# Kernel tuning notes

Measured on AMD Instinct MI355X. Metric: run time of the kernel, lower is better.

Reference implementation:

```python
import jax, jax.numpy as jnp
import numpy as np

E = 8        # n_experts
TOP_K = 2    # top_k_experts


def setup_inputs() -> dict:
    key = jax.random.key(0)
    ks = jax.random.split(key, 4)
    B, N, D, H = 4, 2048, 1024, 1024
    s_d = 1.0 / np.sqrt(D)
    s_h = 1.0 / np.sqrt(H)
    return {
        "x": jax.random.normal(ks[0], (B, N, D), dtype=jnp.float32),
        "router_w": jax.random.normal(ks[1], (E, D), dtype=jnp.float32) * s_d,
        "router_b": jnp.zeros((E,), dtype=jnp.float32),
        "W_up": jax.random.normal(ks[2], (E, D, H), dtype=jnp.float32) * s_d,
        "b_up": jnp.zeros((E, H), dtype=jnp.float32),
        "W_down": jax.random.normal(ks[3], (E, H, D), dtype=jnp.float32) * s_h,
        "b_down": jnp.zeros((E, D), dtype=jnp.float32),
    }


def reference(x, router_w, router_b, W_up, b_up, W_down, b_down):
    # Router logits: (B, N, E)
    logits = jnp.einsum("bnd,ed->bne", x, router_w) + router_b
    _, topk_idx = jax.lax.top_k(logits, TOP_K)          # (B, N, K)
    # Boolean mask of selected experts: (B, N, E)
    mask = jax.nn.one_hot(topk_idx, E, dtype=jnp.bool_).any(axis=-2)
    masked_logits = jnp.where(mask, logits, -jnp.inf)
    router_weights = jax.nn.softmax(masked_logits, axis=-1)  # zeros off top-k
    # Dense all-experts FFN: (B, N, E, H) intermediate
    h = jnp.einsum("bnd,edh->bneh", x, W_up) + b_up
    h = jax.nn.gelu(h, approximate=False)  # torch F.gelu default = exact erf
    h = jnp.einsum("bneh,ehd->bned", h, W_down) + b_down
    output = jnp.einsum("bne,bned->bnd", router_weights, h)
    # Switch load-balancing aux loss (dropout is identity in eval)
    f_i = mask.astype(x.dtype).mean(axis=(0, 1))
    P_i = router_weights.mean(axis=(0, 1))
    aux_loss = E * jnp.sum(f_i * P_i)
    return output, aux_loss
```

## Files before the change

kernel.cpp:

```cpp
#include <hip/hip_runtime.h>
#include <hip/hip_bf16.h>

typedef __attribute__((ext_vector_type(8))) short bf16x8_t;
typedef __attribute__((ext_vector_type(4))) float f32x4_t;

__device__ __forceinline__ void gld16(void* lds, const void* g) {
    __builtin_amdgcn_global_load_lds(
        (const __attribute__((address_space(1))) void*)g,
        (__attribute__((address_space(3))) void*)lds, 16, 0, 0);
}

__device__ inline unsigned short f2bf(float f) {
    __hip_bfloat16 h = __float2bfloat16(f);
    return *reinterpret_cast<unsigned short*>(&h);
}

__global__ __launch_bounds__(256) void transpose_kernel(
    const float* __restrict__ Wup, const float* __restrict__ Wdn,
    ushort* __restrict__ WtUp, ushort* __restrict__ WtDn)
{
    int z = blockIdx.z;
    const float* src = (z < 8) ? (Wup + ((size_t)z << 20)) : (Wdn + ((size_t)(z - 8) << 20));
    ushort* dst      = (z < 8) ? (WtUp + ((size_t)z << 20)) : (WtDn + ((size_t)(z - 8) << 20));
    __shared__ float tile[64][65];
    int x0 = blockIdx.x * 64, y0 = blockIdx.y * 64;
    int row = threadIdx.x >> 4, colq = threadIdx.x & 15;
#pragma unroll
    for (int it = 0; it < 4; it++) {
        int r = row + it * 16;
        float4 v = *(const float4*)(src + (size_t)(y0 + r) * 1024 + x0 + colq * 4);
        tile[r][colq * 4 + 0] = v.x; tile[r][colq * 4 + 1] = v.y;
        tile[r][colq * 4 + 2] = v.z; tile[r][colq * 4 + 3] = v.w;
    }
    __syncthreads();
#pragma unroll
    for (int it = 0; it < 4; it++) {
        int r = row + it * 16;
        ushort4 o;
        o.x = f2bf(tile[colq * 4 + 0][r]); o.y = f2bf(tile[colq * 4 + 1][r]);
        o.z = f2bf(tile[colq * 4 + 2][r]); o.w = f2bf(tile[colq * 4 + 3][r]);
        *(ushort4*)(dst + (size_t)(x0 + r) * 1024 + y0 + colq * 4) = o;
    }
}

__global__ __launch_bounds__(256) void router_kernel(
    const float* __restrict__ x, const float* __restrict__ rw,
    const float* __restrict__ rb, ushort* __restrict__ xb,
    int2* __restrict__ tok_e, float2* __restrict__ tok_w)
{
    int wave = threadIdx.x >> 6, lane = threadIdx.x & 63;
    int t = blockIdx.x * 4 + wave;
    float4 xv[4];
#pragma unroll
    for (int i = 0; i < 4; i++)
        xv[i] = *(const float4*)(x + (size_t)t * 1024 + i * 256 + lane * 4);
#pragma unroll
    for (int i = 0; i < 4; i++) {
        ushort4 o;
        o.x = f2bf(xv[i].x); o.y = f2bf(xv[i].y); o.z = f2bf(xv[i].z); o.w = f2bf(xv[i].w);
        *(ushort4*)(xb + (size_t)t * 1024 + i * 256 + lane * 4) = o;
    }
    float logit[8];
#pragma unroll
    for (int e = 0; e < 8; e++) {
        float s = 0.f;
#pragma unroll
        for (int i = 0; i < 4; i++) {
            float4 wv = *(const float4*)(rw + e * 1024 + i * 256 + lane * 4);
            s += xv[i].x * wv.x + xv[i].y * wv.y + xv[i].z * wv.z + xv[i].w * wv.w;
        }
#pragma unroll
        for (int m = 32; m >= 1; m >>= 1) s += __shfl_xor(s, m, 64);
        logit[e] = s + rb[e];
    }
    int i0 = 0;
#pragma unroll
    for (int e = 1; e < 8; e++) if (logit[e] > logit[i0]) i0 = e;
    int i1 = -1;
#pragma unroll
    for (int e = 0; e < 8; e++) if (e != i0 && (i1 < 0 || logit[e] > logit[i1])) i1 = e;
    float ev = expf(logit[i1] - logit[i0]);
    float s = 1.f + ev;
    if (lane == 0) {
        tok_e[t] = make_int2(i0, i1);
        tok_w[t] = make_float2(1.f / s, ev / s);
    }
}

__global__ __launch_bounds__(256) void count_kernel(
    const int2* __restrict__ tok_e, const float2* __restrict__ tok_w,
    int* __restrict__ blockCnt, float* __restrict__ blockSum)
{
    __shared__ int lcnt[8];
    __shared__ float lsum[8];
    int tid = threadIdx.x;
    if (tid < 8) { lcnt[tid] = 0; lsum[tid] = 0.f; }
    __syncthreads();
    int t = blockIdx.x * 256 + tid;
    int2 e = tok_e[t]; float2 w = tok_w[t];
    atomicAdd(&lcnt[e.x], 1); atomicAdd(&lsum[e.x], w.x);
    atomicAdd(&lcnt[e.y], 1); atomicAdd(&lsum[e.y], w.y);
    __syncthreads();
    if (tid < 8) {
        blockCnt[blockIdx.x * 8 + tid] = lcnt[tid];
        blockSum[blockIdx.x * 8 + tid] = lsum[tid];
    }
}

__global__ void scan_kernel(const int* __restrict__ blockCnt,
                            const float* __restrict__ blockSum,
                            int* __restrict__ cnt, int* __restrict__ off,
                            int* __restrict__ base, int* __restrict__ tileE,
                            int* __restrict__ tileRow, int* __restrict__ nTiles,
                            float* aux_out)
{
    if (threadIdx.x == 0) {
        int tot[8]; float sw[8];
        for (int e = 0; e < 8; e++) { tot[e] = 0; sw[e] = 0.f; }
        for (int b = 0; b < 32; b++)
            for (int e = 0; e < 8; e++) { tot[e] += blockCnt[b * 8 + e]; sw[e] += blockSum[b * 8 + e]; }
        int o = 0; float aux = 0.f; int nT = 0;
        for (int e = 0; e < 8; e++) {
            cnt[e] = tot[e]; off[e] = o;
            aux += (float)tot[e] * sw[e];
            int run = o;
            for (int b = 0; b < 32; b++) { base[b * 8 + e] = run; run += blockCnt[b * 8 + e]; }
            for (int tt = 0; tt * 128 < tot[e]; tt++) { tileE[nT] = e; tileRow[nT] = o + tt * 128; nT++; }
            o += tot[e];
        }
        *nTiles = nT;
        aux *= 8.0f / (8192.0f * 8192.0f);
        *aux_out = aux;
    }
}

__global__ __launch_bounds__(256) void assign_kernel(
    const int2* __restrict__ tok_e, const float2* __restrict__ tok_w,
    const int* __restrict__ base, int* __restrict__ pair_token,
    float* __restrict__ pair_w, int2* __restrict__ tokSlot)
{
    __shared__ int lcnt[8];
    int tid = threadIdx.x;
    if (tid < 8) lcnt[tid] = 0;
    __syncthreads();
    int t = blockIdx.x * 256 + tid;
    int2 e = tok_e[t]; float2 w = tok_w[t];
    int r0 = atomicAdd(&lcnt[e.x], 1);
    int r1 = atomicAdd(&lcnt[e.y], 1);
    int s0 = base[blockIdx.x * 8 + e.x] + r0;
    int s1 = base[blockIdx.x * 8 + e.y] + r1;
    pair_token[s0] = t; pair_w[s0] = w.x;
    pair_token[s1] = t; pair_w[s1] = w.y;
    tokSlot[t] = make_int2(s0, s1);
}

__global__ __launch_bounds__(512, 4) void up_gemm(
    const ushort* __restrict__ xb, const ushort* __restrict__ WtUp,
    const float* __restrict__ bup,
    const int* __restrict__ cnt, const int* __restrict__ off,
    const int* __restrict__ nTiles, const int* __restrict__ tileE,
    const int* __restrict__ tileRow,
    const int* __restrict__ pair_token, const float* __restrict__ pair_w,
    const ushort* __restrict__ zeroPage, ushort* __restrict__ Hbuf)
{
    if ((int)blockIdx.y >= *nTiles) return;
    int e = tileE[blockIdx.y];
    int rowBase = tileRow[blockIdx.y];
    int expertEnd = off[e] + cnt[e];
    int colBase = blockIdx.x * 128;
    const ushort* Bsrc = WtUp + ((size_t)e << 20);

    __shared__ ushort As[128 * 32];
    __shared__ ushort Bs[128 * 32];

    int tid = threadIdx.x, w = tid >> 6, lane = tid & 63;
    int q = lane >> 4, r = lane & 15;
    int wm = w & 3, wn = w >> 2;

    int sr = lane >> 2;
    int cOff = (lane & 3) * 8;
    int rA = w * 16 + sr;
    int gA = rowBase + rA;

    const ushort* aP = (gA < expertEnd) ? xb + (size_t)pair_token[gA] * 1024 + cOff : zeroPage + cOff;
    const ushort* bP = Bsrc + (size_t)(colBase + rA) * 1024 + cOff;

    ushort* lA = &As[(w * 16) * 32];
    ushort* lB = &Bs[(w * 16) * 32];

    f32x4_t acc[2][4];
#pragma unroll
    for (int i = 0; i < 2; i++)
#pragma unroll
        for (int j = 0; j < 4; j++) { acc[i][j][0] = 0.f; acc[i][j][1] = 0.f; acc[i][j][2] = 0.f; acc[i][j][3] = 0.f; }

    for (int kk = 0; kk < 1024; kk += 32) {
        gld16(lA, aP + kk);
        gld16(lB, bP + kk);
        __syncthreads();
        bf16x8_t a[2], b[4];
#pragma unroll
        for (int i = 0; i < 2; i++) a[i] = *(const bf16x8_t*)&As[(wm * 32 + i * 16 + r) * 32 + q * 8];
#pragma unroll
        for (int j = 0; j < 4; j++) b[j] = *(const bf16x8_t*)&Bs[(wn * 64 + j * 16 + r) * 32 + q * 8];
#pragma unroll
        for (int i = 0; i < 2; i++)
#pragma unroll
            for (int j = 0; j < 4; j++)
                acc[i][j] = __builtin_amdgcn_mfma_f32_16x16x32_bf16(a[i], b[j], acc[i][j], 0, 0, 0);
        __syncthreads();
    }

#pragma unroll
    for (int j = 0; j < 4; j++) {
        int col = colBase + wn * 64 + j * 16 + r;
        float bias = bup[e * 1024 + col];
#pragma unroll
        for (int i = 0; i < 2; i++) {
#pragma unroll
            for (int reg = 0; reg < 4; reg++) {
                int gRow = rowBase + wm * 32 + i * 16 + q * 4 + reg;
                if (gRow < expertEnd) {
                    float h = acc[i][j][reg] + bias;
                    float g = 0.5f * h * (1.0f + erff(h * 0.70710678118654752f));
                    Hbuf[(size_t)gRow * 1024 + col] = f2bf(g * pair_w[gRow]);
                }
            }
        }
    }
}

__global__ __launch_bounds__(512, 4) void down_gemm(
    const ushort* __restrict__ Hbuf, const ushort* __restrict__ WtDn,
    const int* __restrict__ cnt, const int* __restrict__ off,
    const int* __restrict__ nTiles, const int* __restrict__ tileE,
    const int* __restrict__ tileRow,
    const ushort* __restrict__ zeroPage, ushort* __restrict__ pairOut)
{
    if ((int)blockIdx.y >= *nTiles) return;
    int e = tileE[blockIdx.y];
    int rowBase = tileRow[blockIdx.y];
    int expertEnd = off[e] + cnt[e];
    int colBase = blockIdx.x * 128;
    const ushort* Bsrc = WtDn + ((size_t)e << 20);

    __shared__ ushort As[128 * 32];
    __shared__ ushort Bs[128 * 32];

    int tid = threadIdx.x, w = tid >> 6, lane = tid & 63;
    int q = lane >> 4, r = lane & 15;
    int wm = w & 3, wn = w >> 2;

    int sr = lane >> 2;
    int cOff = (lane & 3) * 8;
    int rA = w * 16 + sr;
    int gA = rowBase + rA;

    const ushort* aP = (gA < expertEnd) ? Hbuf + (size_t)gA * 1024 + cOff : zeroPage + cOff;
    const ushort* bP = Bsrc + (size_t)(colBase + rA) * 1024 + cOff;

    ushort* lA = &As[(w * 16) * 32];
    ushort* lB = &Bs[(w * 16) * 32];

    f32x4_t acc[2][4];
#pragma unroll
    for (int i = 0; i < 2; i++)
#pragma unroll
        for (int j = 0; j < 4; j++) { acc[i][j][0] = 0.f; acc[i][j][1] = 0.f; acc[i][j][2] = 0.f; acc[i][j][3] = 0.f; }

    for (int kk = 0; kk < 1024; kk += 32) {
        gld16(lA, aP + kk);
        gld16(lB, bP + kk);
        __syncthreads();
        bf16x8_t a[2], b[4];
#pragma unroll
        for (int i = 0; i < 2; i++) a[i] = *(const bf16x8_t*)&As[(wm * 32 + i * 16 + r) * 32 + q * 8];
#pragma unroll
        for (int j = 0; j < 4; j++) b[j] = *(const bf16x8_t*)&Bs[(wn * 64 + j * 16 + r) * 32 + q * 8];
#pragma unroll
        for (int i = 0; i < 2; i++)
#pragma unroll
            for (int j = 0; j < 4; j++)
                acc[i][j] = __builtin_amdgcn_mfma_f32_16x16x32_bf16(a[i], b[j], acc[i][j], 0, 0, 0);
        __syncthreads();
    }

#pragma unroll
    for (int j = 0; j < 4; j++) {
        int col = colBase + wn * 64 + j * 16 + r;
#pragma unroll
        for (int i = 0; i < 2; i++) {
#pragma unroll
            for (int reg = 0; reg < 4; reg++) {
                int gRow = rowBase + wm * 32 + i * 16 + q * 4 + reg;
                if (gRow < expertEnd)
                    pairOut[(size_t)gRow * 1024 + col] = f2bf(acc[i][j][reg]);
            }
        }
    }
}

__global__ __launch_bounds__(256) void finalize_kernel(
    const ushort* __restrict__ pairOut, const int2* __restrict__ tokSlot,
    const int2* __restrict__ tok_e, const float2* __restrict__ tok_w,
    const float* __restrict__ bdn, float* __restrict__ out)
{
    int t = blockIdx.x;
    int2 s = tokSlot[t]; int2 e = tok_e[t]; float2 w = tok_w[t];
    int c = threadIdx.x * 4;
    ushort4 p0 = *(const ushort4*)(pairOut + (size_t)s.x * 1024 + c);
    ushort4 p1 = *(const ushort4*)(pairOut + (size_t)s.y * 1024 + c);
    float4 b0 = *(const float4*)(bdn + (size_t)e.x * 1024 + c);
    float4 b1 = *(const float4*)(bdn + (size_t)e.y * 1024 + c);
    __hip_bfloat16* h0 = (__hip_bfloat16*)&p0;
    __hip_bfloat16* h1 = (__hip_bfloat16*)&p1;
    float4 o;
    o.x = __bfloat162float(h0[0]) + __bfloat162float(h1[0]) + w.x * b0.x + w.y * b1.x;
    o.y = __bfloat162float(h0[1]) + __bfloat162float(h1[1]) + w.x * b0.y + w.y * b1.y;
    o.z = __bfloat162float(h0[2]) + __bfloat162float(h1[2]) + w.x * b0.z + w.y * b1.z;
    o.w = __bfloat162float(h0[3]) + __bfloat162float(h1[3]) + w.x * b0.w + w.y * b1.w;
    *(float4*)(out + (size_t)t * 1024 + c) = o;
}

extern "C" void kernel_launch(void* const* d_in, const int* in_sizes, int n_in,
                              void* d_out, int out_size, void* d_ws, size_t ws_size,
                              hipStream_t stream) {
    const float* x   = (const float*)d_in[0];
    const float* rw  = (const float*)d_in[1];
    const float* rb  = (const float*)d_in[2];
    const float* Wup = (const float*)d_in[3];
    const float* bup = (const float*)d_in[4];
    const float* Wdn = (const float*)d_in[5];
    const float* bdn = (const float*)d_in[6];
    float* out = (float*)d_out;

    char* ws = (char*)d_ws;
    int*    cnt      = (int*)(ws + 0);
    int*    off      = (int*)(ws + 64);
    int*    nTiles   = (int*)(ws + 128);
    int*    blockCnt = (int*)(ws + 256);
    float*  blockSum = (float*)(ws + 1536);
    int*    base     = (int*)(ws + 2816);
    int*    tileE    = (int*)(ws + 4096);
    int*    tileRow  = (int*)(ws + 4736);
    ushort* zeroPage = (ushort*)(ws + 8192);
    int2*   tok_e    = (int2*)(ws + 12288);
    float2* tok_w    = (float2*)(ws + 77824);
    int2*   tokSlot  = (int2*)(ws + 143360);
    int*    pair_token = (int*)(ws + 208896);
    float*  pair_w     = (float*)(ws + 274432);
    char* big = ws + 1048576;
    ushort* Hbuf    = (ushort*)big;
    ushort* pairOut = (ushort*)(big + 33554432);
    ushort* WtUp    = (ushort*)(big + 67108864);
    ushort* WtDn    = (ushort*)(big + 83886080);
    ushort* xb      = (ushort*)(big + 100663296);

    hipMemsetAsync(zeroPage, 0, 4096, stream);

    transpose_kernel<<<dim3(16, 16, 16), 256, 0, stream>>>(Wup, Wdn, WtUp, WtDn);
    router_kernel<<<2048, 256, 0, stream>>>(x, rw, rb, xb, tok_e, tok_w);
    count_kernel<<<32, 256, 0, stream>>>(tok_e, tok_w, blockCnt, blockSum);
    scan_kernel<<<1, 64, 0, stream>>>(blockCnt, blockSum, cnt, off, base,
                                      tileE, tileRow, nTiles, out + 8388608);
    assign_kernel<<<32, 256, 0, stream>>>(tok_e, tok_w, base, pair_token, pair_w, tokSlot);
    up_gemm<<<dim3(8, 136), 512, 0, stream>>>(
        xb, WtUp, bup, cnt, off, nTiles, tileE, tileRow, pair_token, pair_w, zeroPage, Hbuf);
    down_gemm<<<dim3(8, 136), 512, 0, stream>>>(
        Hbuf, WtDn, cnt, off, nTiles, tileE, tileRow, zeroPage, pairOut);
    finalize_kernel<<<8192, 256, 0, stream>>>(pairOut, tokSlot, tok_e, tok_w, bdn, out);
}
```

Measured before the change: 344.4 us.

## Switch expert GEMMs to 32x32x16 MFMA with 4-wave blocks and K=64 tiles

Both grouped GEMMs now use 256-thread blocks of 4 waves, each computing a 64x64 sub-tile with 32x32x16 bf16 MFMA instead of 16x16x32. K steps double to 64 per LDS stage, which halves the barrier count, and the LDS layout is arranged in MFMA-fragment order so each lane reads its operand with one contiguous vector load. The aim is higher MFMA throughput per LDS read and less sync overhead. The costs are more accumulator registers per thread and fewer waves per block to hide latency. An empty unused template helper is also added.

```diff
diff --git a/kernel.cpp b/kernel.cpp
--- a/kernel.cpp
+++ b/kernel.cpp
@@ -2,7 +2,7 @@
 #include <hip/hip_bf16.h>
 
 typedef __attribute__((ext_vector_type(8))) short bf16x8_t;
-typedef __attribute__((ext_vector_type(4))) float f32x4_t;
+typedef __attribute__((ext_vector_type(16))) float f32x16_t;
 
 __device__ __forceinline__ void gld16(void* lds, const void* g) {
     __builtin_amdgcn_global_load_lds(
@@ -154,7 +154,13 @@
     tokSlot[t] = make_int2(s0, s1);
 }
 
-__global__ __launch_bounds__(512, 4) void up_gemm(
+
+template <bool UP>
+__device__ __forceinline__ void gemm128_body(
+    const ushort* __restrict__ Asrc_rows[],
+    int dummy) {}
+
+__global__ __launch_bounds__(256, 4) void up_gemm(
     const ushort* __restrict__ xb, const ushort* __restrict__ WtUp,
     const float* __restrict__ bup,
     const int* __restrict__ cnt, const int* __restrict__ off,
@@ -170,67 +176,74 @@
     int colBase = blockIdx.x * 128;
     const ushort* Bsrc = WtUp + ((size_t)e << 20);
 
-    __shared__ ushort As[128 * 32];
-    __shared__ ushort Bs[128 * 32];
+    __shared__ ushort As[128 * 64];
+    __shared__ ushort Bs[128 * 64];
 
     int tid = threadIdx.x, w = tid >> 6, lane = tid & 63;
-    int q = lane >> 4, r = lane & 15;
-    int wm = w & 3, wn = w >> 2;
-
-    int sr = lane >> 2;
-    int cOff = (lane & 3) * 8;
-    int rA = w * 16 + sr;
-    int gA = rowBase + rA;
-
-    const ushort* aP = (gA < expertEnd) ? xb + (size_t)pair_token[gA] * 1024 + cOff : zeroPage + cOff;
-    const ushort* bP = Bsrc + (size_t)(colBase + rA) * 1024 + cOff;
-
-    ushort* lA = &As[(w * 16) * 32];
-    ushort* lB = &Bs[(w * 16) * 32];
-
-    f32x4_t acc[2][4];
+    int half = lane >> 5, m = lane & 31;
+    int wm = w & 1, wn = w >> 1;
+
+    int gA = rowBase + w * 32 + m;
+    const ushort* aRow = (gA < expertEnd) ? xb + (size_t)pair_token[gA] * 1024 : zeroPage;
+    const ushort* aP = aRow + half * 8;
+    const ushort* bP = Bsrc + (size_t)(colBase + w * 32 + m) * 1024 + half * 8;
+    ushort* lA = &As[w * 2048];
+    ushort* lB = &Bs[w * 2048];
+
+    f32x16_t acc[2][2];
 #pragma unroll
     for (int i = 0; i < 2; i++)
 #pragma unroll
-        for (int j = 0; j < 4; j++) { acc[i][j][0] = 0.f; acc[i][j][1] = 0.f; acc[i][j][2] = 0.f; acc[i][j][3] = 0.f; }
-
-    for (int kk = 0; kk < 1024; kk += 32) {
-        gld16(lA, aP + kk);
-        gld16(lB, bP + kk);
+        for (int j = 0; j < 2; j++)
+#pragma unroll
+            for (int p = 0; p < 16; p++) acc[i][j][p] = 0.f;
+
+    for (int kk = 0; kk < 1024; kk += 64) {
+#pragma unroll
+        for (int j = 0; j < 4; j++) {
+            gld16(lA + j * 512, aP + kk + j * 16);
+            gld16(lB + j * 512, bP + kk + j * 16);
+        }
         __syncthreads();
-        bf16x8_t a[2], b[4];
-#pragma unroll
-        for (int i = 0; i < 2; i++) a[i] = *(const bf16x8_t*)&As[(wm * 32 + i * 16 + r) * 32 + q * 8];
-#pragma unroll
-        for (int j = 0; j < 4; j++) b[j] = *(const bf16x8_t*)&Bs[(wn * 64 + j * 16 + r) * 32 + q * 8];
-#pragma unroll
-        for (int i = 0; i < 2; i++)
-#pragma unroll
-            for (int j = 0; j < 4; j++)
-                acc[i][j] = __builtin_amdgcn_mfma_f32_16x16x32_bf16(a[i], b[j], acc[i][j], 0, 0, 0);
+#pragma unroll
+        for (int s = 0; s < 4; s++) {
+            bf16x8_t a[2], b[2];
+#pragma unroll
+            for (int i = 0; i < 2; i++)
+                a[i] = *(const bf16x8_t*)&As[(((wm * 2 + i) * 4 + s) * 64 + lane) * 8];
+#pragma unroll
+            for (int j = 0; j < 2; j++)
+                b[j] = *(const bf16x8_t*)&Bs[(((wn * 2 + j) * 4 + s) * 64 + lane) * 8];
+#pragma unroll
+            for (int i = 0; i < 2; i++)
+#pragma unroll
+                for (int j = 0; j < 2; j++)
+                    acc[i][j] = __builtin_amdgcn_mfma_f32_32x32x16_bf16(a[i], b[j], acc[i][j], 0, 0, 0);
+        }
         __syncthreads();
     }
 
 #pragma unroll
-    for (int j = 0; j < 4; j++) {
-        int col = colBase + wn * 64 + j * 16 + r;
-        float bias = bup[e * 1024 + col];
-#pragma unroll
-        for (int i = 0; i < 2; i++) {
-#pragma unroll
-            for (int reg = 0; reg < 4; reg++) {
-                int gRow = rowBase + wm * 32 + i * 16 + q * 4 + reg;
-                if (gRow < expertEnd) {
-                    float h = acc[i][j][reg] + bias;
+    for (int i = 0; i < 2; i++) {
+#pragma unroll
+        for (int p = 0; p < 16; p++) {
+            int rl = (p & 3) + 8 * (p >> 2) + 4 * half;
+            int gRow = rowBase + (wm * 2 + i) * 32 + rl;
+            if (gRow < expertEnd) {
+                float wgt = pair_w[gRow];
+#pragma unroll
+                for (int j = 0; j < 2; j++) {
+                    int col = colBase + (wn * 2 + j) * 32 + m;
+                    float h = acc[i][j][p] + bup[e * 1024 + col];
                     float g = 0.5f * h * (1.0f + erff(h * 0.70710678118654752f));
-                    Hbuf[(size_t)gRow * 1024 + col] = f2bf(g * pair_w[gRow]);
+                    Hbuf[(size_t)gRow * 1024 + col] = f2bf(g * wgt);
                 }
             }
         }
     }
 }
 
-__global__ __launch_bounds__(512, 4) void down_gemm(
+__global__ __launch_bounds__(256, 4) void down_gemm(
     const ushort* __restrict__ Hbuf, const ushort* __restrict__ WtDn,
     const int* __restrict__ cnt, const int* __restrict__ off,
     const int* __restrict__ nTiles, const int* __restrict__ tileE,
@@ -244,57 +257,65 @@
     int colBase = blockIdx.x * 128;
     const ushort* Bsrc = WtDn + ((size_t)e << 20);
 
-    __shared__ ushort As[128 * 32];
-    __shared__ ushort Bs[128 * 32];
+    __shared__ ushort As[128 * 64];
+    __shared__ ushort Bs[128 * 64];
 
     int tid = threadIdx.x, w = tid >> 6, lane = tid & 63;
-    int q = lane >> 4, r = lane & 15;
-    int wm = w & 3, wn = w >> 2;
-
-    int sr = lane >> 2;
-    int cOff = (lane & 3) * 8;
-    int rA = w * 16 + sr;
-    int gA = rowBase + rA;
-
-    const ushort* aP = (gA < expertEnd) ? Hbuf + (size_t)gA * 1024 + cOff : zeroPage + cOff;
-    const ushort* bP = Bsrc + (size_t)(colBase + rA) * 1024 + cOff;
-
-    ushort* lA = &As[(w * 16) * 32];
-    ushort* lB = &Bs[(w * 16) * 32];
-
-    f32x4_t acc[2][4];
+    int half = lane >> 5, m = lane & 31;
+    int wm = w & 1, wn = w >> 1;
+
+    int gA = rowBase + w * 32 + m;
+    const ushort* aRow = (gA < expertEnd) ? Hbuf + (size_t)gA * 1024 : zeroPage;
+    const ushort* aP = aRow + half * 8;
+    const ushort* bP = Bsrc + (size_t)(colBase + w * 32 + m) * 1024 + half * 8;
+    ushort* lA = &As[w * 2048];
+    ushort* lB = &Bs[w * 2048];
+
+    f32x16_t acc[2][2];
 #pragma unroll
     for (int i = 0; i < 2; i++)
 #pragma unroll
-        for (int j = 0; j < 4; j++) { acc[i][j][0] = 0.f; acc[i][j][1] = 0.f; acc[i][j][2] = 0.f; acc[i][j][3] = 0.f; }
-
-    for (int kk = 0; kk < 1024; kk += 32) {
-        gld16(lA, aP + kk);
-        gld16(lB, bP + kk);
+        for (int j = 0; j < 2; j++)
+#pragma unroll
+            for (int p = 0; p < 16; p++) acc[i][j][p] = 0.f;
+
+    for (int kk = 0; kk < 1024; kk += 64) {
+#pragma unroll
+        for (int j = 0; j < 4; j++) {
+            gld16(lA + j * 512, aP + kk + j * 16);
+            gld16(lB + j * 512, bP + kk + j * 16);
+        }
         __syncthreads();
-        bf16x8_t a[2], b[4];
-#pragma unroll
-        for (int i = 0; i < 2; i++) a[i] = *(const bf16x8_t*)&As[(wm * 32 + i * 16 + r) * 32 + q * 8];
-#pragma unroll
-        for (int j = 0; j < 4; j++) b[j] = *(const bf16x8_t*)&Bs[(wn * 64 + j * 16 + r) * 32 + q * 8];
-#pragma unroll
-        for (int i = 0; i < 2; i++)
-#pragma unroll
-            for (int j = 0; j < 4; j++)
-                acc[i][j] = __builtin_amdgcn_mfma_f32_16x16x32_bf16(a[i], b[j], acc[i][j], 0, 0, 0);
+#pragma unroll
+        for (int s = 0; s < 4; s++) {
+            bf16x8_t a[2], b[2];
+#pragma unroll
+            for (int i = 0; i < 2; i++)
+                a[i] = *(const bf16x8_t*)&As[(((wm * 2 + i) * 4 + s) * 64 + lane) * 8];
+#pragma unroll
+            for (int j = 0; j < 2; j++)
+                b[j] = *(const bf16x8_t*)&Bs[(((wn * 2 + j) * 4 + s) * 64 + lane) * 8];
+#pragma unroll
+            for (int i = 0; i < 2; i++)
+#pragma unroll
+                for (int j = 0; j < 2; j++)
+                    acc[i][j] = __builtin_amdgcn_mfma_f32_32x32x16_bf16(a[i], b[j], acc[i][j], 0, 0, 0);
+        }
         __syncthreads();
     }
 
 #pragma unroll
-    for (int j = 0; j < 4; j++) {
-        int col = colBase + wn * 64 + j * 16 + r;
-#pragma unroll
-        for (int i = 0; i < 2; i++) {
-#pragma unroll
-            for (int reg = 0; reg < 4; reg++) {
-                int gRow = rowBase + wm * 32 + i * 16 + q * 4 + reg;
-                if (gRow < expertEnd)
-                    pairOut[(size_t)gRow * 1024 + col] = f2bf(acc[i][j][reg]);
+    for (int i = 0; i < 2; i++) {
+#pragma unroll
+        for (int p = 0; p < 16; p++) {
+            int rl = (p & 3) + 8 * (p >> 2) + 4 * half;
+            int gRow = rowBase + (wm * 2 + i) * 32 + rl;
+            if (gRow < expertEnd) {
+#pragma unroll
+                for (int j = 0; j < 2; j++) {
+                    int col = colBase + (wn * 2 + j) * 32 + m;
+                    pairOut[(size_t)gRow * 1024 + col] = f2bf(acc[i][j][p]);
+                }
             }
         }
     }
@@ -364,9 +385,9 @@
     scan_kernel<<<1, 64, 0, stream>>>(blockCnt, blockSum, cnt, off, base,
                                       tileE, tileRow, nTiles, out + 8388608);
     assign_kernel<<<32, 256, 0, stream>>>(tok_e, tok_w, base, pair_token, pair_w, tokSlot);
-    up_gemm<<<dim3(8, 136), 512, 0, stream>>>(
+    up_gemm<<<dim3(8, 136), 256, 0, stream>>>(
         xb, WtUp, bup, cnt, off, nTiles, tileE, tileRow, pair_token, pair_w, zeroPage, Hbuf);
-    down_gemm<<<dim3(8, 136), 512, 0, stream>>>(
+    down_gemm<<<dim3(8, 136), 256, 0, stream>>>(
         Hbuf, WtDn, cnt, off, nTiles, tileE, tileRow, zeroPage, pairOut);
     finalize_kernel<<<8192, 256, 0, stream>>>(pairOut, tokSlot, tok_e, tok_w, bdn, out);
 }
```

Measured after the change: 399.0 us. 15.8% more time.

## Swizzle LDS tiles, use tanh GELU, fold down bias into GEMM epilogue

Applied to the files above, without the earlier changes.

XOR-swizzles the 16-byte chunks of each LDS row in both expert GEMMs so that MFMA operand reads hit different banks, aiming to reduce LDS bank conflicts. Replaces the erf-based GELU with a tanh/exp approximation to cut epilogue cost, at the price of small numerical deviation from the exact GELU. Moves the weighted down-projection bias add into the down_gemm epilogue so the finalize kernel reads less data.

```diff
diff --git a/kernel.cpp b/kernel.cpp
--- a/kernel.cpp
+++ b/kernel.cpp
@@ -13,6 +13,11 @@
 __device__ inline unsigned short f2bf(float f) {
     __hip_bfloat16 h = __float2bfloat16(f);
     return *reinterpret_cast<unsigned short*>(&h);
+}
+
+__device__ __forceinline__ float gelu_fast(float h) {
+    float u = 0.7978845608028654f * h * (1.0f + 0.044715f * h * h);
+    return h / (1.0f + __expf(-2.0f * u));
 }
 
 __global__ __launch_bounds__(256) void transpose_kernel(
@@ -154,6 +159,7 @@
     tokSlot[t] = make_int2(s0, s1);
 }
 
+
 __global__ __launch_bounds__(512, 4) void up_gemm(
     const ushort* __restrict__ xb, const ushort* __restrict__ WtUp,
     const float* __restrict__ bup,
@@ -178,15 +184,16 @@
     int wm = w & 3, wn = w >> 2;
 
     int sr = lane >> 2;
-    int cOff = (lane & 3) * 8;
-    int rA = w * 16 + sr;
-    int gA = rowBase + rA;
+    int rowL = w * 16 + sr;
+    int qg = (lane & 3) ^ (sr & 3);
+    int cOff = qg * 8;
+    int gA = rowBase + rowL;
 
     const ushort* aP = (gA < expertEnd) ? xb + (size_t)pair_token[gA] * 1024 + cOff : zeroPage + cOff;
-    const ushort* bP = Bsrc + (size_t)(colBase + rA) * 1024 + cOff;
-
-    ushort* lA = &As[(w * 16) * 32];
-    ushort* lB = &Bs[(w * 16) * 32];
+    const ushort* bP = Bsrc + (size_t)(colBase + rowL) * 1024 + cOff;
+
+    ushort* lA = &As[w * 512];
+    ushort* lB = &Bs[w * 512];
 
     f32x4_t acc[2][4];
 #pragma unroll
@@ -200,9 +207,15 @@
         __syncthreads();
         bf16x8_t a[2], b[4];
 #pragma unroll
-        for (int i = 0; i < 2; i++) a[i] = *(const bf16x8_t*)&As[(wm * 32 + i * 16 + r) * 32 + q * 8];
-#pragma unroll
-        for (int j = 0; j < 4; j++) b[j] = *(const bf16x8_t*)&Bs[(wn * 64 + j * 16 + r) * 32 + q * 8];
+        for (int i = 0; i < 2; i++) {
+            int ra = wm * 32 + i * 16 + r;
+            a[i] = *(const bf16x8_t*)&As[ra * 32 + ((q ^ (ra & 3)) * 8)];
+        }
+#pragma unroll
+        for (int j = 0; j < 4; j++) {
+            int rb2 = wn * 64 + j * 16 + r;
+            b[j] = *(const bf16x8_t*)&Bs[rb2 * 32 + ((q ^ (rb2 & 3)) * 8)];
+        }
 #pragma unroll
         for (int i = 0; i < 2; i++)
 #pragma unroll
@@ -222,8 +235,7 @@
                 int gRow = rowBase + wm * 32 + i * 16 + q * 4 + reg;
                 if (gRow < expertEnd) {
                     float h = acc[i][j][reg] + bias;
-                    float g = 0.5f * h * (1.0f + erff(h * 0.70710678118654752f));
-                    Hbuf[(size_t)gRow * 1024 + col] = f2bf(g * pair_w[gRow]);
+                    Hbuf[(size_t)gRow * 1024 + col] = f2bf(gelu_fast(h) * pair_w[gRow]);
                 }
             }
         }
@@ -232,9 +244,10 @@
 
 __global__ __launch_bounds__(512, 4) void down_gemm(
     const ushort* __restrict__ Hbuf, const ushort* __restrict__ WtDn,
+    const float* __restrict__ bdn,
     const int* __restrict__ cnt, const int* __restrict__ off,
     const int* __restrict__ nTiles, const int* __restrict__ tileE,
-    const int* __restrict__ tileRow,
+    const int* __restrict__ tileRow, const float* __restrict__ pair_w,
     const ushort* __restrict__ zeroPage, ushort* __restrict__ pairOut)
 {
     if ((int)blockIdx.y >= *nTiles) return;
@@ -252,15 +265,16 @@
     int wm = w & 3, wn = w >> 2;
 
     int sr = lane >> 2;
-    int cOff = (lane & 3) * 8;
-    int rA = w * 16 + sr;
-    int gA = rowBase + rA;
+    int rowL = w * 16 + sr;
+    int qg = (lane & 3) ^ (sr & 3);
+    int cOff = qg * 8;
+    int gA = rowBase + rowL;
 
     const ushort* aP = (gA < expertEnd) ? Hbuf + (size_t)gA * 1024 + cOff : zeroPage + cOff;
-    const ushort* bP = Bsrc + (size_t)(colBase + rA) * 1024 + cOff;
-
-    ushort* lA = &As[(w * 16) * 32];
-    ushort* lB = &Bs[(w * 16) * 32];
+    const ushort* bP = Bsrc + (size_t)(colBase + rowL) * 1024 + cOff;
+
+    ushort* lA = &As[w * 512];
+    ushort* lB = &Bs[w * 512];
 
     f32x4_t acc[2][4];
 #pragma unroll
@@ -274,9 +288,15 @@
         __syncthreads();
         bf16x8_t a[2], b[4];
 #pragma unroll
-        for (int i = 0; i < 2; i++) a[i] = *(const bf16x8_t*)&As[(wm * 32 + i * 16 + r) * 32 + q * 8];
-#pragma unroll
-        for (int j = 0; j < 4; j++) b[j] = *(const bf16x8_t*)&Bs[(wn * 64 + j * 16 + r) * 32 + q * 8];
+        for (int i = 0; i < 2; i++) {
+            int ra = wm * 32 + i * 16 + r;
+            a[i] = *(const bf16x8_t*)&As[ra * 32 + ((q ^ (ra & 3)) * 8)];
+        }
+#pragma unroll
+        for (int j = 0; j < 4; j++) {
+            int rb2 = wn * 64 + j * 16 + r;
+            b[j] = *(const bf16x8_t*)&Bs[rb2 * 32 + ((q ^ (rb2 & 3)) * 8)];
+        }
 #pragma unroll
         for (int i = 0; i < 2; i++)
 #pragma unroll
@@ -288,13 +308,14 @@
 #pragma unroll
     for (int j = 0; j < 4; j++) {
         int col = colBase + wn * 64 + j * 16 + r;
+        float bias = bdn[e * 1024 + col];
 #pragma unroll
         for (int i = 0; i < 2; i++) {
 #pragma unroll
             for (int reg = 0; reg < 4; reg++) {
                 int gRow = rowBase + wm * 32 + i * 16 + q * 4 + reg;
                 if (gRow < expertEnd)
-                    pairOut[(size_t)gRow * 1024 + col] = f2bf(acc[i][j][reg]);
+                    pairOut[(size_t)gRow * 1024 + col] = f2bf(acc[i][j][reg] + pair_w[gRow] * bias);
             }
         }
     }
@@ -302,23 +323,20 @@
 
 __global__ __launch_bounds__(256) void finalize_kernel(
     const ushort* __restrict__ pairOut, const int2* __restrict__ tokSlot,
-    const int2* __restrict__ tok_e, const float2* __restrict__ tok_w,
-    const float* __restrict__ bdn, float* __restrict__ out)
+    float* __restrict__ out)
 {
     int t = blockIdx.x;
-    int2 s = tokSlot[t]; int2 e = tok_e[t]; float2 w = tok_w[t];
+    int2 s = tokSlot[t];
     int c = threadIdx.x * 4;
     ushort4 p0 = *(const ushort4*)(pairOut + (size_t)s.x * 1024 + c);
     ushort4 p1 = *(const ushort4*)(pairOut + (size_t)s.y * 1024 + c);
-    float4 b0 = *(const float4*)(bdn + (size_t)e.x * 1024 + c);
-    float4 b1 = *(const float4*)(bdn + (size_t)e.y * 1024 + c);
     __hip_bfloat16* h0 = (__hip_bfloat16*)&p0;
     __hip_bfloat16* h1 = (__hip_bfloat16*)&p1;
     float4 o;
-    o.x = __bfloat162float(h0[0]) + __bfloat162float(h1[0]) + w.x * b0.x + w.y * b1.x;
-    o.y = __bfloat162float(h0[1]) + __bfloat162float(h1[1]) + w.x * b0.y + w.y * b1.y;
-    o.z = __bfloat162float(h0[2]) + __bfloat162float(h1[2]) + w.x * b0.z + w.y * b1.z;
-    o.w = __bfloat162float(h0[3]) + __bfloat162float(h1[3]) + w.x * b0.w + w.y * b1.w;
+    o.x = __bfloat162float(h0[0]) + __bfloat162float(h1[0]);
+    o.y = __bfloat162float(h0[1]) + __bfloat162float(h1[1]);
+    o.z = __bfloat162float(h0[2]) + __bfloat162float(h1[2]);
+    o.w = __bfloat162float(h0[3]) + __bfloat162float(h1[3]);
     *(float4*)(out + (size_t)t * 1024 + c) = o;
 }
 
@@ -367,6 +385,6 @@
     up_gemm<<<dim3(8, 136), 512, 0, stream>>>(
         xb, WtUp, bup, cnt, off, nTiles, tileE, tileRow, pair_token, pair_w, zeroPage, Hbuf);
     down_gemm<<<dim3(8, 136), 512, 0, stream>>>(
-        Hbuf, WtDn, cnt, off, nTiles, tileE, tileRow, zeroPage, pairOut);
-    finalize_kernel<<<8192, 256, 0, stream>>>(pairOut, tokSlot, tok_e, tok_w, bdn, out);
-}
+        Hbuf, WtDn, bdn, cnt, off, nTiles, tileE, tileRow, pair_w, zeroPage, pairOut);
+    finalize_kernel<<<8192, 256, 0, stream>>>(pairOut, tokSlot, out);
+}
```

New measurement: 345.4 us. About the same (+0.3%).
